# Kernel tuning notes

Hardware: AMD Instinct MI355X
Metric: run time of the kernel (lower is better)

Reference implementation:

```python
import jax, jax.numpy as jnp
import numpy as np


def _layernorm(x, g, b, eps=1e-5):
    m = x.mean(-1, keepdims=True)
    v = ((x - m) ** 2).mean(-1, keepdims=True)
    return (x - m) * jax.lax.rsqrt(v + eps) * g + b


def setup_inputs() -> dict:
    key = jax.random.key(0)
    ks = jax.random.split(key, 12)
    B, V, E, N = 8, 64, 512, 32          # batch, num_vars, embed(=input_dim), num_samples
    L, H, D, M, R = 4, 8, 64, 1024, 128  # layers, heads, head_dim, mlp_dim, resolution
    HD = H * D
    s = 0.02
    return {
        "flow_encoded": jax.random.normal(ks[0], (B, V, E), jnp.float32),
        "W_shift": s * jax.random.normal(ks[1], (E, HD), jnp.float32),
        "b_shift": jnp.zeros((HD,), jnp.float32),
        "Wk": s * jax.random.normal(ks[2], (L, H, E, D), jnp.float32),
        "bk": jnp.zeros((L, H, D), jnp.float32),
        "Wv": s * jax.random.normal(ks[3], (L, H, E, D), jnp.float32),
        "bv": jnp.zeros((L, H, D), jnp.float32),
        "ln1_g": jnp.ones((L, HD), jnp.float32),
        "ln1_b": jnp.zeros((L, HD), jnp.float32),
        "W1": s * jax.random.normal(ks[4], (L, HD, M), jnp.float32),
        "b1": jnp.zeros((L, M), jnp.float32),
        "W2": s * jax.random.normal(ks[5], (L, M, M), jnp.float32),
        "b2": jnp.zeros((L, M), jnp.float32),
        "W3": s * jax.random.normal(ks[6], (L, M, HD), jnp.float32),
        "b3": jnp.zeros((L, HD), jnp.float32),
        "ln2_g": jnp.ones((L, HD), jnp.float32),
        "ln2_b": jnp.zeros((L, HD), jnp.float32),
        "W_dist": s * jax.random.normal(ks[7], (HD, R), jnp.float32),
        "b_dist": jnp.zeros((R,), jnp.float32),
        "num_samples": N,
    }


def _forward_logits(flow_encoded, W_shift, b_shift, Wk, bk, Wv, bv,
                    ln1_g, ln1_b, W1, b1, W2, b2, W3, b3, ln2_g, ln2_b,
                    W_dist, b_dist, num_samples):
    B, V, E = flow_encoded.shape
    L, H, _, D = Wk.shape
    HD = H * D
    # history keys/values: all heads in one einsum (replaces per-head nn.Linear loop)
    keys = jnp.einsum('bve,lhed->lbhvd', flow_encoded, Wk) + bk[:, None, :, None, :]
    vals = jnp.einsum('bve,lhed->lbhvd', flow_encoded, Wv) + bv[:, None, :, None, :]
    # queries per (var, sample); vectorized over vars (outer loop in source is independent)
    att = flow_encoded @ W_shift + b_shift                      # [B, V, HD]
    att = jnp.broadcast_to(att[:, :, None, :], (B, V, num_samples, HD))
    scale = D ** -0.5
    for l in range(L):
        q = att.reshape(B, V, num_samples, H, D)
        scores = jnp.einsum('bvnhd,bhwd->bvnhw', q, keys[l]) * scale
        w = jax.nn.softmax(scores, axis=-1)
        a = jnp.einsum('bvnhw,bhwd->bvnhd', w, vals[l]).reshape(B, V, num_samples, HD)
        att = _layernorm(att + a, ln1_g[l], ln1_b[l])
        h = jax.nn.relu(att @ W1[l] + b1[l])
        h = jax.nn.relu(h @ W2[l] + b2[l])
        h = h @ W3[l] + b3[l]
        att = _layernorm(att + h, ln2_g[l], ln2_b[l])
    return att @ W_dist + b_dist                                # [B, V, N, R]


def reference(flow_encoded, W_shift, b_shift, Wk, bk, Wv, bv,
              ln1_g, ln1_b, W1, b1, W2, b2, W3, b3, ln2_g, ln2_b,
              W_dist, b_dist, num_samples):
    logits = _forward_logits(flow_encoded, W_shift, b_shift, Wk, bk, Wv, bv,
                             ln1_g, ln1_b, W1, b1, W2, b2, W3, b3, ln2_g, ln2_b,
                             W_dist, b_dist, num_samples)
    R = b_dist.shape[0]
    k = jax.random.key(1)
    idx = jax.random.categorical(jax.random.fold_in(k, 0), logits, axis=-1)  # multinomial(1)
    u = jax.random.uniform(jax.random.fold_in(k, 1), idx.shape, jnp.float32)
    samples = (idx.astype(jnp.float32) + u) / R                 # [B, V, N]
    return samples
```

## Files before the change

### kernel.cpp

```cpp
#include <hip/hip_runtime.h>
#include <hip/hip_bf16.h>
#include <math.h>

constexpr int B  = 8,  V = 64, E = 512, NS = 32;
constexpr int L  = 4,  H = 8,  D = 64,  M  = 1024, R = 128;
constexpr int HD = H * D;
constexpr int ROWS  = B * V;
constexpr int SROWS = ROWS * NS;
constexpr int KVN = 4096;

typedef _Float16 half8 __attribute__((ext_vector_type(8)));
typedef float floatx4 __attribute__((ext_vector_type(4)));

struct TF2 { unsigned a, b; };
__host__ __device__ constexpr unsigned rotl32(unsigned x, int d) {
  return (x << d) | (x >> (32 - d));
}
__host__ __device__ constexpr TF2 threefry(unsigned k0, unsigned k1,
                                           unsigned x0, unsigned x1) {
  unsigned ks2 = k0 ^ k1 ^ 0x1BD11BDAu;
  x0 += k0; x1 += k1;
  const int ra[4] = {13, 15, 26, 6};
  const int rb[4] = {17, 29, 16, 24};
  for (int i = 0; i < 4; i++) { x0 += x1; x1 = rotl32(x1, ra[i]); x1 ^= x0; }
  x0 += k1;  x1 += ks2 + 1u;
  for (int i = 0; i < 4; i++) { x0 += x1; x1 = rotl32(x1, rb[i]); x1 ^= x0; }
  x0 += ks2; x1 += k0 + 2u;
  for (int i = 0; i < 4; i++) { x0 += x1; x1 = rotl32(x1, ra[i]); x1 ^= x0; }
  x0 += k0;  x1 += k1 + 3u;
  for (int i = 0; i < 4; i++) { x0 += x1; x1 = rotl32(x1, rb[i]); x1 ^= x0; }
  x0 += k1;  x1 += ks2 + 4u;
  for (int i = 0; i < 4; i++) { x0 += x1; x1 = rotl32(x1, ra[i]); x1 ^= x0; }
  x0 += ks2; x1 += k0 + 5u;
  return {x0, x1};
}
__device__ __forceinline__ unsigned tf_bits32(unsigned k0, unsigned k1,
                                              unsigned j) {
  TF2 r = threefry(k0, k1, 0u, j);
  return r.a ^ r.b;
}

__device__ __forceinline__ double waveReduceAdd64(double v) {
#pragma unroll
  for (int m = 32; m; m >>= 1) v += __shfl_xor(v, m, 64);
  return v;
}

__device__ __forceinline__ void split16(float v, _Float16& h, _Float16& l) {
  h = (_Float16)v;
  l = (_Float16)((v - (float)h) * 2048.0f);
}

__global__ __launch_bounds__(256) void prep_kernel(
    const float* __restrict__ flow, const float* __restrict__ bk,
    const float* __restrict__ bv, const float* __restrict__ bsh,
    _Float16* __restrict__ fh, _Float16* __restrict__ fl,
    float* __restrict__ h3, float* __restrict__ logits,
    float* __restrict__ kvb) {
  const int blk = blockIdx.x, t = threadIdx.x;
  if (blk < 256) {
    const int base = (blk * 256 + t) * 4;
    float4 v = *(const float4*)&flow[base];
    float a[4] = {v.x, v.y, v.z, v.w};
#pragma unroll
    for (int j = 0; j < 4; j++) {
      _Float16 h, l;
      split16(a[j], h, l);
      fh[base + j] = h;
      fl[base + j] = l;
    }
  } else if (blk < 512) {
    const int idx = (blk - 256) * 256 + t;
    float4 z = {0.f, 0.f, 0.f, 0.f};
    *(float4*)&h3[idx * 4] = z;
    if (idx < KVN + HD) {
      float bb = (idx < 2048) ? bk[idx]
               : (idx < 4096) ? bv[idx - 2048]
                              : bsh[idx - 4096];
      kvb[idx] = bb;
    }
  } else {
    const int idx = (blk - 512) * 256 + t;
    float4 z = {0.f, 0.f, 0.f, 0.f};
    *(float4*)&logits[idx * 4] = z;
  }
}

struct WArgs {
  const float* s[7];
  _Float16* h[7];
  _Float16* l[7];
};
__global__ __launch_bounds__(256) void wsplit_all(WArgs a) {
  const int WS_OFF[8] = {0, 64, 320, 576, 1088, 2112, 2624, 2640};
  const int WS_K[7] = {512, 512, 512, 512, 1024, 1024, 512};
  const int WS_N[7] = {512, 64, 64, 1024, 1024, 512, 128};
  __shared__ float tile[64][65];
  int bid = blockIdx.x;
  int mi = 0;
  while (bid >= WS_OFF[mi + 1]) mi++;
  int tt = bid - WS_OFF[mi];
  const int K = WS_K[mi], N = WS_N[mi];
  const int ktiles = K >> 6;
  const int per = ktiles * (N >> 6);
  const int z = tt / per;
  const int rem = tt - z * per;
  const int k0 = (rem % ktiles) * 64, n0 = (rem / ktiles) * 64;
  const size_t moff = (size_t)z * K * N;
  const float* src = a.s[mi] + moff;
  _Float16* dh = a.h[mi] + moff;
  _Float16* dl = a.l[mi] + moff;
  const int t = threadIdx.x;
#pragma unroll
  for (int i = 0; i < 16; i++) {
    int idx = i * 256 + t, r = idx >> 6, c = idx & 63;
    tile[r][c] = src[(size_t)(k0 + r) * N + n0 + c];
  }
  __syncthreads();
#pragma unroll
  for (int i = 0; i < 16; i++) {
    int idx = i * 256 + t, n = idx >> 6, k = idx & 63;
    float v = tile[k][n];
    _Float16 h, l;
    split16(v, h, l);
    dh[(size_t)(n0 + n) * K + k0 + k] = h;
    dl[(size_t)(n0 + n) * K + k0 + k] = l;
  }
}

__global__ __launch_bounds__(256) void mfma_gemm(
    const _Float16* __restrict__ Ah, const _Float16* __restrict__ Al,
    const _Float16* __restrict__ Bh, const _Float16* __restrict__ Bl,
    const float* __restrict__ bias, float* __restrict__ C0, int ldc0,
    float* __restrict__ C1, int ldc1, int nsplit,
    _Float16* __restrict__ Oh, _Float16* __restrict__ Ol, int K, int relu,
    int kz) {
  __shared__ __align__(16) _Float16 lds[2 * 8192];
  const int t = threadIdx.x;
  const int lane = t & 63, wave = t >> 6;
  const int quad = lane >> 4, l15 = lane & 15;
  const int m0 = blockIdx.x * 32, n0 = blockIdx.y * 32;
  const int kchunk = K / kz, kbase = blockIdx.z * kchunk;
  const int KT = kchunk >> 6;
  const _Float16* srcs[4] = {Ah + (size_t)m0 * K, Al + (size_t)m0 * K,
                             Bh + (size_t)n0 * K, Bl + (size_t)n0 * K};
  const _Float16* gsrc = srcs[wave];
  auto stage = [&](int buf, int kt) {
    _Float16* base = &lds[buf * 8192 + wave * 2048];
    const int kcol = kbase + kt * 64 + quad * 8;
#pragma unroll
    for (int r = 0; r < 2; r++)
#pragma unroll
      for (int s = 0; s < 2; s++)
        __builtin_amdgcn_global_load_lds(
            gsrc + (size_t)(r * 16 + l15) * K + kcol + s * 32,
            base + (r * 2 + s) * 512, 16, 0, 0);
  };
  const int wm = wave >> 1, wn = wave & 1;
  floatx4 hh = {0.f, 0.f, 0.f, 0.f};
  floatx4 mid = {0.f, 0.f, 0.f, 0.f};
  stage(0, 0);
  __syncthreads();
  for (int kt = 0; kt < KT; kt++) {
    if (kt + 1 < KT) stage((kt + 1) & 1, kt + 1);
    const int b = (kt & 1) * 8192;
#pragma unroll
    for (int s = 0; s < 2; s++) {
      const int afr = (wm * 2 + s) * 512 + lane * 8;
      const int bfr = (wn * 2 + s) * 512 + lane * 8;
      half8 a_h = *(const half8*)&lds[b + afr];
      half8 a_l = *(const half8*)&lds[b + 2048 + afr];
      half8 b_h = *(const half8*)&lds[b + 4096 + bfr];
      half8 b_l = *(const half8*)&lds[b + 6144 + bfr];
      hh = __builtin_amdgcn_mfma_f32_16x16x32_f16(a_h, b_h, hh, 0, 0, 0);
      mid = __builtin_amdgcn_mfma_f32_16x16x32_f16(a_h, b_l, mid, 0, 0, 0);
      mid = __builtin_amdgcn_mfma_f32_16x16x32_f16(a_l, b_h, mid, 0, 0, 0);
    }
    __syncthreads();
  }
#pragma unroll
  for (int r = 0; r < 4; r++) {
    float v = hh[r] + mid[r] * (1.0f / 2048.0f);
    const int m = m0 + wm * 16 + quad * 4 + r;
    const int n = n0 + wn * 16 + l15;
    if (kz == 1) {
      v += bias[n];
      if (relu) v = fmaxf(v, 0.0f);
      if (n < nsplit) {
        if (C0) C0[(size_t)m * ldc0 + n] = v;
        if (Oh) {
          _Float16 h, l;
          split16(v, h, l);
          Oh[(size_t)m * ldc0 + n] = h;
          Ol[(size_t)m * ldc0 + n] = l;
        }
      } else {
        C1[(size_t)m * ldc1 + (n - nsplit)] = v;
      }
    } else {
      if (blockIdx.z == 0) v += bias[n];
      atomicAdd(&C0[(size_t)m * ldc0 + n], v);
    }
  }
}

__global__ __launch_bounds__(256) void attn_kernel(
    float* __restrict__ att, _Float16* __restrict__ att_h,
    _Float16* __restrict__ att_l, const float* __restrict__ kv,
    const float* __restrict__ g, const float* __restrict__ bb, int l) {
  __shared__ float q[HD];
  __shared__ float sp[HD];
  __shared__ double rb[8];
  const int t = threadIdx.x;
  const int row = blockIdx.x;
  const int b_ = row >> 6;
  q[t]       = att[row * HD + t];
  q[t + 256] = att[row * HD + 256 + t];
  __syncthreads();
#pragma unroll
  for (int rep = 0; rep < 2; rep++) {
    int idx = t + rep * 256;
    int h = idx >> 6, w = idx & 63;
    const float* kp = kv + (size_t)(b_ * 64 + w) * KVN + (l * 8 + h) * 64;
    const float* qp = q + h * D;
    double s = 0.0;
#pragma unroll 8
    for (int d = 0; d < 64; d++) s += (double)qp[d] * (double)kp[d];
    sp[idx] = (float)s * 0.125f;
  }
  __syncthreads();
  {
    int h = t >> 5, w0 = t & 31;
    float s0 = sp[h * 64 + w0], s1 = sp[h * 64 + w0 + 32];
    float mx = fmaxf(s0, s1);
#pragma unroll
    for (int m = 16; m; m >>= 1) mx = fmaxf(mx, __shfl_xor(mx, m, 32));
    float e0 = expf(s0 - mx), e1 = expf(s1 - mx);
    double sm = (double)e0 + (double)e1;
#pragma unroll
    for (int m = 16; m; m >>= 1) sm += __shfl_xor(sm, m, 32);
    sp[h * 64 + w0]      = (float)((double)e0 / sm);
    sp[h * 64 + w0 + 32] = (float)((double)e1 / sm);
  }
  __syncthreads();
  float x[2];
#pragma unroll
  for (int rep = 0; rep < 2; rep++) {
    int idx = t + rep * 256;
    int h = idx >> 6, d = idx & 63;
    const float* vp = kv + (size_t)(b_ * 64) * KVN + 2048 + (l * 8 + h) * 64 + d;
    const float* pp = sp + h * 64;
    double a = 0.0;
#pragma unroll 8
    for (int w = 0; w < 64; w++) a += (double)pp[w] * (double)vp[(size_t)w * KVN];
    x[rep] = q[idx] + (float)a;
  }
  double s1 = (double)x[0] + (double)x[1];
  double s2 = (double)x[0] * (double)x[0] + (double)x[1] * (double)x[1];
  s1 = waveReduceAdd64(s1);
  s2 = waveReduceAdd64(s2);
  const int wid = t >> 6, lane = t & 63;
  if (lane == 0) { rb[wid] = s1; rb[4 + wid] = s2; }
  __syncthreads();
  double S1 = rb[0] + rb[1] + rb[2] + rb[3];
  double S2 = rb[4] + rb[5] + rb[6] + rb[7];
  double mean = S1 / (double)HD;
  double var  = S2 / (double)HD - mean * mean;
  double inv  = 1.0 / sqrt(var + (double)1e-5f);
  float y0 =
      (float)(((double)x[0] - mean) * inv * (double)g[t] + (double)bb[t]);
  float y1 = (float)(((double)x[1] - mean) * inv * (double)g[t + 256] +
                     (double)bb[t + 256]);
  att[row * HD + t] = y0;
  att[row * HD + 256 + t] = y1;
  _Float16 h0, l0, h1v, l1v;
  split16(y0, h0, l0);
  split16(y1, h1v, l1v);
  att_h[row * HD + t] = h0;
  att_l[row * HD + t] = l0;
  att_h[row * HD + 256 + t] = h1v;
  att_l[row * HD + 256 + t] = l1v;
}

__global__ __launch_bounds__(256) void ln_res_kernel(
    float* __restrict__ att, _Float16* __restrict__ att_h,
    _Float16* __restrict__ att_l, float* __restrict__ h3,
    const float* __restrict__ g, const float* __restrict__ bb) {
  __shared__ double rb[8];
  const int t = threadIdx.x;
  const int row = blockIdx.x;
  float x0 = att[row * HD + t] + h3[row * HD + t];
  float x1 = att[row * HD + 256 + t] + h3[row * HD + 256 + t];
  h3[row * HD + t] = 0.0f;
  h3[row * HD + 256 + t] = 0.0f;
  double s1 = (double)x0 + (double)x1;
  double s2 = (double)x0 * (double)x0 + (double)x1 * (double)x1;
  s1 = waveReduceAdd64(s1);
  s2 = waveReduceAdd64(s2);
  const int wid = t >> 6, lane = t & 63;
  if (lane == 0) { rb[wid] = s1; rb[4 + wid] = s2; }
  __syncthreads();
  double S1 = rb[0] + rb[1] + rb[2] + rb[3];
  double S2 = rb[4] + rb[5] + rb[6] + rb[7];
  double mean = S1 / (double)HD;
  double var  = S2 / (double)HD - mean * mean;
  double inv  = 1.0 / sqrt(var + (double)1e-5f);
  float y0 = (float)(((double)x0 - mean) * inv * (double)g[t] + (double)bb[t]);
  float y1 = (float)(((double)x1 - mean) * inv * (double)g[t + 256] +
                     (double)bb[t + 256]);
  att[row * HD + t] = y0;
  att[row * HD + 256 + t] = y1;
  _Float16 h0, l0, h1v, l1v;
  split16(y0, h0, l0);
  split16(y1, h1v, l1v);
  att_h[row * HD + t] = h0;
  att_l[row * HD + t] = l0;
  att_h[row * HD + 256 + t] = h1v;
  att_l[row * HD + 256 + t] = l1v;
}

__global__ __launch_bounds__(256) void sample_kernel(
    const float* __restrict__ logits, float* __restrict__ out) {
  constexpr TF2 KC = threefry(0u, 1u, 0u, 0u);
  constexpr TF2 KU = threefry(0u, 1u, 0u, 1u);
  const int lane = threadIdx.x & 63;
  const int wid = threadIdx.x >> 6;
  const int row = blockIdx.x * 4 + wid;
  const float* lrow = logits + (row >> 5) * R;
  float bvv = -1e30f;
  int bi = 0;
#pragma unroll
  for (int rep = 0; rep < 2; rep++) {
    int r = lane + rep * 64;
    unsigned j = (unsigned)row * (unsigned)R + (unsigned)r;
    unsigned bits = tf_bits32(KC.a, KC.b, j);
    float f = __uint_as_float((bits >> 9) | 0x3f800000u) - 1.0f;
    float u = fmaxf(f, 1.17549435e-38f);
    float gv = -logf(-logf(u));
    float v = lrow[r] + gv;
    if (v > bvv) { bvv = v; bi = r; }
  }
#pragma unroll
  for (int m = 32; m; m >>= 1) {
    float ov = __shfl_xor(bvv, m, 64);
    int oi = __shfl_xor(bi, m, 64);
    if (ov > bvv || (ov == bvv && oi < bi)) { bvv = ov; bi = oi; }
  }
  if (lane == 0) {
    unsigned ub = tf_bits32(KU.a, KU.b, (unsigned)row);
    float u = __uint_as_float((ub >> 9) | 0x3f800000u) - 1.0f;
    out[row] = ((float)bi + u) * (1.0f / 128.0f);
  }
}

extern "C" void kernel_launch(void* const* d_in, const int* in_sizes, int n_in,
                              void* d_out, int out_size, void* d_ws,
                              size_t ws_size, hipStream_t stream) {
  (void)in_sizes; (void)n_in; (void)out_size; (void)ws_size;
  const float* flow = (const float*)d_in[0];
  const float* Wsh  = (const float*)d_in[1];
  const float* bsh  = (const float*)d_in[2];
  const float* Wk   = (const float*)d_in[3];
  const float* bk   = (const float*)d_in[4];
  const float* Wv   = (const float*)d_in[5];
  const float* bv   = (const float*)d_in[6];
  const float* ln1g = (const float*)d_in[7];
  const float* ln1b = (const float*)d_in[8];
  const float* W1   = (const float*)d_in[9];
  const float* b1   = (const float*)d_in[10];
  const float* W2   = (const float*)d_in[11];
  const float* b2   = (const float*)d_in[12];
  const float* W3   = (const float*)d_in[13];
  const float* b3   = (const float*)d_in[14];
  const float* ln2g = (const float*)d_in[15];
  const float* ln2b = (const float*)d_in[16];
  const float* Wd   = (const float*)d_in[17];
  const float* bd   = (const float*)d_in[18];

  float* ws = (float*)d_ws;
  float* kv     = ws;
  float* att    = kv + ROWS * KVN;
  float* h3     = att + ROWS * HD;
  float* logits = h3 + ROWS * HD;
  float* kvb    = logits + ROWS * R;
  _Float16* hp = (_Float16*)(kvb + 4608);
  _Float16* flow_h = hp;            hp += 262144;
  _Float16* flow_l = hp;            hp += 262144;
  _Float16* BKV_h  = hp;            hp += 4608 * 512;
  _Float16* BKV_l  = hp;            hp += 4608 * 512;
  _Float16* W1_h   = hp;            hp += 2097152;
  _Float16* W1_l   = hp;            hp += 2097152;
  _Float16* W2_h   = hp;            hp += 4194304;
  _Float16* W2_l   = hp;            hp += 4194304;
  _Float16* W3_h   = hp;            hp += 2097152;
  _Float16* W3_l   = hp;            hp += 2097152;
  _Float16* Wd_h   = hp;            hp += 65536;
  _Float16* Wd_l   = hp;            hp += 65536;
  _Float16* att_h  = hp;            hp += 262144;
  _Float16* att_l  = hp;            hp += 262144;
  _Float16* h1_h   = hp;            hp += 524288;
  _Float16* h1_l   = hp;            hp += 524288;
  _Float16* h2_h   = hp;            hp += 524288;
  _Float16* h2_l   = hp;            hp += 524288;

  const int NSPLIT_NONE = 1 << 30;

  prep_kernel<<<576, 256, 0, stream>>>(flow, bk, bv, bsh, flow_h, flow_l, h3,
                                       logits, kvb);
  WArgs wa;
  wa.s[0] = Wsh; wa.h[0] = BKV_h + 4096 * 512; wa.l[0] = BKV_l + 4096 * 512;
  wa.s[1] = Wk;  wa.h[1] = BKV_h;              wa.l[1] = BKV_l;
  wa.s[2] = Wv;  wa.h[2] = BKV_h + 2048 * 512; wa.l[2] = BKV_l + 2048 * 512;
  wa.s[3] = W1;  wa.h[3] = W1_h;  wa.l[3] = W1_l;
  wa.s[4] = W2;  wa.h[4] = W2_h;  wa.l[4] = W2_l;
  wa.s[5] = W3;  wa.h[5] = W3_h;  wa.l[5] = W3_l;
  wa.s[6] = Wd;  wa.h[6] = Wd_h;  wa.l[6] = Wd_l;
  wsplit_all<<<2640, 256, 0, stream>>>(wa);

  mfma_gemm<<<dim3(16, 144, 1), 256, 0, stream>>>(
      flow_h, flow_l, BKV_h, BKV_l, kvb, kv, KVN, att, HD, KVN, nullptr,
      nullptr, 512, 0, 1);

  for (int l = 0; l < L; l++) {
    attn_kernel<<<ROWS, 256, 0, stream>>>(att, att_h, att_l, kv, ln1g + l * HD,
                                          ln1b + l * HD, l);
    mfma_gemm<<<dim3(16, 32, 1), 256, 0, stream>>>(
        att_h, att_l, W1_h + (size_t)l * 524288, W1_l + (size_t)l * 524288,
        b1 + l * M, nullptr, M, nullptr, 0, NSPLIT_NONE, h1_h, h1_l, 512, 1,
        1);
    mfma_gemm<<<dim3(16, 32, 1), 256, 0, stream>>>(
        h1_h, h1_l, W2_h + (size_t)l * 1048576, W2_l + (size_t)l * 1048576,
        b2 + l * M, nullptr, M, nullptr, 0, NSPLIT_NONE, h2_h, h2_l, 1024, 1,
        1);
    mfma_gemm<<<dim3(16, 16, 2), 256, 0, stream>>>(
        h2_h, h2_l, W3_h + (size_t)l * 524288, W3_l + (size_t)l * 524288,
        b3 + l * HD, h3, HD, nullptr, 0, NSPLIT_NONE, nullptr, nullptr, 1024,
        0, 2);
    ln_res_kernel<<<ROWS, 256, 0, stream>>>(att, att_h, att_l, h3,
                                            ln2g + l * HD, ln2b + l * HD);
  }
  mfma_gemm<<<dim3(16, 4, 2), 256, 0, stream>>>(
      att_h, att_l, Wd_h, Wd_l, bd, logits, R, nullptr, 0, NSPLIT_NONE,
      nullptr, nullptr, 512, 0, 2);
  sample_kernel<<<SROWS / 4, 256, 0, stream>>>(logits, (float*)d_out);
}
```

Measured before the change: 435.8 us.

## Load MFMA operands straight from global memory, drop split-K atomics and zeroing

The GEMM kernel stops staging A/B tiles through double-buffered LDS with global_load_lds. Each wave now loads its own 16-row fragments directly from global memory into registers, prefetching the next K-step in software. Split-K with atomicAdd is removed, so the W3 and logits GEMMs write results directly, and the h3 and logits buffers no longer need zero-initialising in prep or resetting in ln_res. The grid is transposed so blockIdx.x walks N, which changes which blocks share operand rows. The trade-off is that operands are no longer shared between waves through LDS, so global and L2 traffic goes up. The split-K GEMMs also lose parallelism because they now launch half as many blocks.

```diff
diff --git a/kernel.cpp b/kernel.cpp
--- a/kernel.cpp
+++ b/kernel.cpp
@@ -55,7 +55,6 @@
     const float* __restrict__ flow, const float* __restrict__ bk,
     const float* __restrict__ bv, const float* __restrict__ bsh,
     _Float16* __restrict__ fh, _Float16* __restrict__ fl,
-    float* __restrict__ h3, float* __restrict__ logits,
     float* __restrict__ kvb) {
   const int blk = blockIdx.x, t = threadIdx.x;
   if (blk < 256) {
@@ -69,20 +68,14 @@
       fh[base + j] = h;
       fl[base + j] = l;
     }
-  } else if (blk < 512) {
+  } else {
     const int idx = (blk - 256) * 256 + t;
-    float4 z = {0.f, 0.f, 0.f, 0.f};
-    *(float4*)&h3[idx * 4] = z;
     if (idx < KVN + HD) {
       float bb = (idx < 2048) ? bk[idx]
                : (idx < 4096) ? bv[idx - 2048]
                               : bsh[idx - 4096];
       kvb[idx] = bb;
     }
-  } else {
-    const int idx = (blk - 512) * 256 + t;
-    float4 z = {0.f, 0.f, 0.f, 0.f};
-    *(float4*)&logits[idx * 4] = z;
   }
 }
 
@@ -133,73 +126,56 @@
     const _Float16* __restrict__ Bh, const _Float16* __restrict__ Bl,
     const float* __restrict__ bias, float* __restrict__ C0, int ldc0,
     float* __restrict__ C1, int ldc1, int nsplit,
-    _Float16* __restrict__ Oh, _Float16* __restrict__ Ol, int K, int relu,
-    int kz) {
-  __shared__ __align__(16) _Float16 lds[2 * 8192];
-  const int t = threadIdx.x;
-  const int lane = t & 63, wave = t >> 6;
+    _Float16* __restrict__ Oh, _Float16* __restrict__ Ol, int K, int relu) {
+  const int t = threadIdx.x, lane = t & 63, wave = t >> 6;
   const int quad = lane >> 4, l15 = lane & 15;
-  const int m0 = blockIdx.x * 32, n0 = blockIdx.y * 32;
-  const int kchunk = K / kz, kbase = blockIdx.z * kchunk;
-  const int KT = kchunk >> 6;
-  const _Float16* srcs[4] = {Ah + (size_t)m0 * K, Al + (size_t)m0 * K,
-                             Bh + (size_t)n0 * K, Bl + (size_t)n0 * K};
-  const _Float16* gsrc = srcs[wave];
-  auto stage = [&](int buf, int kt) {
-    _Float16* base = &lds[buf * 8192 + wave * 2048];
-    const int kcol = kbase + kt * 64 + quad * 8;
-#pragma unroll
-    for (int r = 0; r < 2; r++)
-#pragma unroll
-      for (int s = 0; s < 2; s++)
-        __builtin_amdgcn_global_load_lds(
-            gsrc + (size_t)(r * 16 + l15) * K + kcol + s * 32,
-            base + (r * 2 + s) * 512, 16, 0, 0);
-  };
+  const int n0 = blockIdx.x * 32, m0 = blockIdx.y * 32;
   const int wm = wave >> 1, wn = wave & 1;
+  const size_t aoff = (size_t)(m0 + wm * 16 + l15) * K + quad * 8;
+  const size_t boff = (size_t)(n0 + wn * 16 + l15) * K + quad * 8;
+  const _Float16* pAh = Ah + aoff;
+  const _Float16* pAl = Al + aoff;
+  const _Float16* pBh = Bh + boff;
+  const _Float16* pBl = Bl + boff;
   floatx4 hh = {0.f, 0.f, 0.f, 0.f};
   floatx4 mid = {0.f, 0.f, 0.f, 0.f};
-  stage(0, 0);
-  __syncthreads();
+  const int KT = K >> 5;
+  half8 ca = *(const half8*)&pAh[0];
+  half8 cal = *(const half8*)&pAl[0];
+  half8 cb = *(const half8*)&pBh[0];
+  half8 cbl = *(const half8*)&pBl[0];
+  half8 na = ca, nal = cal, nb = cb, nbl = cbl;
+#pragma unroll 4
   for (int kt = 0; kt < KT; kt++) {
-    if (kt + 1 < KT) stage((kt + 1) & 1, kt + 1);
-    const int b = (kt & 1) * 8192;
-#pragma unroll
-    for (int s = 0; s < 2; s++) {
-      const int afr = (wm * 2 + s) * 512 + lane * 8;
-      const int bfr = (wn * 2 + s) * 512 + lane * 8;
-      half8 a_h = *(const half8*)&lds[b + afr];
-      half8 a_l = *(const half8*)&lds[b + 2048 + afr];
-      half8 b_h = *(const half8*)&lds[b + 4096 + bfr];
-      half8 b_l = *(const half8*)&lds[b + 6144 + bfr];
-      hh = __builtin_amdgcn_mfma_f32_16x16x32_f16(a_h, b_h, hh, 0, 0, 0);
-      mid = __builtin_amdgcn_mfma_f32_16x16x32_f16(a_h, b_l, mid, 0, 0, 0);
-      mid = __builtin_amdgcn_mfma_f32_16x16x32_f16(a_l, b_h, mid, 0, 0, 0);
+    const int kn = (kt + 1) << 5;
+    if (kt + 1 < KT) {
+      na = *(const half8*)&pAh[kn];
+      nal = *(const half8*)&pAl[kn];
+      nb = *(const half8*)&pBh[kn];
+      nbl = *(const half8*)&pBl[kn];
     }
-    __syncthreads();
+    hh = __builtin_amdgcn_mfma_f32_16x16x32_f16(ca, cb, hh, 0, 0, 0);
+    mid = __builtin_amdgcn_mfma_f32_16x16x32_f16(ca, cbl, mid, 0, 0, 0);
+    mid = __builtin_amdgcn_mfma_f32_16x16x32_f16(cal, cb, mid, 0, 0, 0);
+    ca = na; cal = nal; cb = nb; cbl = nbl;
   }
 #pragma unroll
   for (int r = 0; r < 4; r++) {
     float v = hh[r] + mid[r] * (1.0f / 2048.0f);
     const int m = m0 + wm * 16 + quad * 4 + r;
     const int n = n0 + wn * 16 + l15;
-    if (kz == 1) {
-      v += bias[n];
-      if (relu) v = fmaxf(v, 0.0f);
-      if (n < nsplit) {
-        if (C0) C0[(size_t)m * ldc0 + n] = v;
-        if (Oh) {
-          _Float16 h, l;
-          split16(v, h, l);
-          Oh[(size_t)m * ldc0 + n] = h;
-          Ol[(size_t)m * ldc0 + n] = l;
-        }
-      } else {
-        C1[(size_t)m * ldc1 + (n - nsplit)] = v;
+    v += bias[n];
+    if (relu) v = fmaxf(v, 0.0f);
+    if (n < nsplit) {
+      if (C0) C0[(size_t)m * ldc0 + n] = v;
+      if (Oh) {
+        _Float16 h, l;
+        split16(v, h, l);
+        Oh[(size_t)m * ldc0 + n] = h;
+        Ol[(size_t)m * ldc0 + n] = l;
       }
     } else {
-      if (blockIdx.z == 0) v += bias[n];
-      atomicAdd(&C0[(size_t)m * ldc0 + n], v);
+      C1[(size_t)m * ldc1 + (n - nsplit)] = v;
     }
   }
 }
@@ -284,15 +260,13 @@
 
 __global__ __launch_bounds__(256) void ln_res_kernel(
     float* __restrict__ att, _Float16* __restrict__ att_h,
-    _Float16* __restrict__ att_l, float* __restrict__ h3,
+    _Float16* __restrict__ att_l, const float* __restrict__ h3,
     const float* __restrict__ g, const float* __restrict__ bb) {
   __shared__ double rb[8];
   const int t = threadIdx.x;
   const int row = blockIdx.x;
   float x0 = att[row * HD + t] + h3[row * HD + t];
   float x1 = att[row * HD + 256 + t] + h3[row * HD + 256 + t];
-  h3[row * HD + t] = 0.0f;
-  h3[row * HD + 256 + t] = 0.0f;
   double s1 = (double)x0 + (double)x1;
   double s2 = (double)x0 * (double)x0 + (double)x1 * (double)x1;
   s1 = waveReduceAdd64(s1);
@@ -405,8 +379,7 @@
 
   const int NSPLIT_NONE = 1 << 30;
 
-  prep_kernel<<<576, 256, 0, stream>>>(flow, bk, bv, bsh, flow_h, flow_l, h3,
-                                       logits, kvb);
+  prep_kernel<<<275, 256, 0, stream>>>(flow, bk, bv, bsh, flow_h, flow_l, kvb);
   WArgs wa;
   wa.s[0] = Wsh; wa.h[0] = BKV_h + 4096 * 512; wa.l[0] = BKV_l + 4096 * 512;
   wa.s[1] = Wk;  wa.h[1] = BKV_h;              wa.l[1] = BKV_l;
@@ -417,30 +390,28 @@
   wa.s[6] = Wd;  wa.h[6] = Wd_h;  wa.l[6] = Wd_l;
   wsplit_all<<<2640, 256, 0, stream>>>(wa);
 
-  mfma_gemm<<<dim3(16, 144, 1), 256, 0, stream>>>(
+  mfma_gemm<<<dim3(144, 16), 256, 0, stream>>>(
       flow_h, flow_l, BKV_h, BKV_l, kvb, kv, KVN, att, HD, KVN, nullptr,
-      nullptr, 512, 0, 1);
+      nullptr, 512, 0);
 
   for (int l = 0; l < L; l++) {
     attn_kernel<<<ROWS, 256, 0, stream>>>(att, att_h, att_l, kv, ln1g + l * HD,
                                           ln1b + l * HD, l);
-    mfma_gemm<<<dim3(16, 32, 1), 256, 0, stream>>>(
+    mfma_gemm<<<dim3(32, 16), 256, 0, stream>>>(
         att_h, att_l, W1_h + (size_t)l * 524288, W1_l + (size_t)l * 524288,
-        b1 + l * M, nullptr, M, nullptr, 0, NSPLIT_NONE, h1_h, h1_l, 512, 1,
-        1);
-    mfma_gemm<<<dim3(16, 32, 1), 256, 0, stream>>>(
+        b1 + l * M, nullptr, M, nullptr, 0, NSPLIT_NONE, h1_h, h1_l, 512, 1);
+    mfma_gemm<<<dim3(32, 16), 256, 0, stream>>>(
         h1_h, h1_l, W2_h + (size_t)l * 1048576, W2_l + (size_t)l * 1048576,
-        b2 + l * M, nullptr, M, nullptr, 0, NSPLIT_NONE, h2_h, h2_l, 1024, 1,
-        1);
-    mfma_gemm<<<dim3(16, 16, 2), 256, 0, stream>>>(
+        b2 + l * M, nullptr, M, nullptr, 0, NSPLIT_NONE, h2_h, h2_l, 1024, 1);
+    mfma_gemm<<<dim3(16, 16), 256, 0, stream>>>(
         h2_h, h2_l, W3_h + (size_t)l * 524288, W3_l + (size_t)l * 524288,
         b3 + l * HD, h3, HD, nullptr, 0, NSPLIT_NONE, nullptr, nullptr, 1024,
-        0, 2);
+        0);
     ln_res_kernel<<<ROWS, 256, 0, stream>>>(att, att_h, att_l, h3,
                                             ln2g + l * HD, ln2b + l * HD);
   }
-  mfma_gemm<<<dim3(16, 4, 2), 256, 0, stream>>>(
+  mfma_gemm<<<dim3(4, 16), 256, 0, stream>>>(
       att_h, att_l, Wd_h, Wd_l, bd, logits, R, nullptr, 0, NSPLIT_NONE,
-      nullptr, nullptr, 512, 0, 2);
+      nullptr, nullptr, 512, 0);
   sample_kernel<<<SROWS / 4, 256, 0, stream>>>(logits, (float*)d_out);
 }
```

New measurement: 562.5 us. 29.1% more time.
